# Kernel tuning notes

Hardware: AMD Instinct MI355X
Metric: run time of the kernel (lower is better)

Reference implementation:

```python
import jax, jax.numpy as jnp
import numpy as np

N_NODES = 100000
N_EDGES = 1600000
IN_CH, HID_CH, OUT_CH = 128, 64, 40
NEG_SLOPE = 0.2  # PyG GATConv default LeakyReLU slope


def setup_inputs() -> dict:
    key = jax.random.key(0)
    ks = jax.random.split(key, 12)
    x = jax.random.normal(ks[0], (N_NODES, IN_CH), dtype=jnp.float32)
    src = jax.random.randint(ks[1], (N_EDGES,), 0, N_NODES)
    dst = jax.random.randint(ks[2], (N_EDGES,), 0, N_NODES)
    # remove accidental self loops so that add_remaining_self_loops == append arange
    dst = jnp.where(src == dst, (dst + 1) % N_NODES, dst)
    edge_index = jnp.stack([src, dst], axis=0).astype(jnp.int64)
    s1 = 1.0 / np.sqrt(IN_CH)
    s2 = 1.0 / np.sqrt(HID_CH)
    return {
        "x": x,
        "edge_index": edge_index,
        "W1": jax.random.normal(ks[3], (IN_CH, HID_CH), dtype=jnp.float32) * s1,
        "a_src1": jax.random.normal(ks[4], (HID_CH,), dtype=jnp.float32) * s2,
        "a_dst1": jax.random.normal(ks[5], (HID_CH,), dtype=jnp.float32) * s2,
        "b1": jnp.zeros((HID_CH,), dtype=jnp.float32),
        "W2": jax.random.normal(ks[6], (HID_CH, OUT_CH), dtype=jnp.float32) * s2,
        "a_src2": jax.random.normal(ks[7], (OUT_CH,), dtype=jnp.float32) / np.sqrt(OUT_CH),
        "a_dst2": jax.random.normal(ks[8], (OUT_CH,), dtype=jnp.float32) / np.sqrt(OUT_CH),
        "b2": jnp.zeros((OUT_CH,), dtype=jnp.float32),
    }


def _gat_conv(x, src, dst, W, a_src, a_dst, b, n_nodes):
    # h: [N, F_out] transformed features
    h = x @ W
    # per-node attention logits (heads=1): alpha_src[n] = <h[n], a_src>
    al_src = h @ a_src  # [N]
    al_dst = h @ a_dst  # [N]
    # edge-wise gather + LeakyReLU
    e = al_src[src] + al_dst[dst]          # [E]
    e = jnp.where(e > 0, e, NEG_SLOPE * e)
    # softmax over incoming edges of each destination node
    m = jax.ops.segment_max(e, dst, num_segments=n_nodes)   # [N]
    w = jnp.exp(e - m[dst])                                  # [E]
    z = jax.ops.segment_sum(w, dst, num_segments=n_nodes)    # [N]
    alpha = w / (z[dst] + 1e-16)                              # [E]
    # weighted scatter of neighbor features
    out = jax.ops.segment_sum(h[src] * alpha[:, None], dst, num_segments=n_nodes)
    return out + b


def reference(x, edge_index, W1, a_src1, a_dst1, b1, W2, a_src2, a_dst2, b2):
    n = x.shape[0]
    # add_remaining_self_loops: edges were built with no self loops
    loops = jnp.arange(n, dtype=edge_index.dtype)
    src = jnp.concatenate([edge_index[0], loops])
    dst = jnp.concatenate([edge_index[1], loops])
    h = _gat_conv(x, src, dst, W1, a_src1, a_dst1, b1, n)
    h = jax.nn.relu(h)  # dropout is identity in eval mode
    out = _gat_conv(h, src, dst, W2, a_src2, a_dst2, b2, n)
    return jax.nn.log_softmax(out, axis=1)
```

## Files before the change

kernel.cpp:

```cpp
#include <hip/hip_runtime.h>
#include <hip/hip_fp16.h>

#define N_NODES 100000
#define N_EDGESC 1600000
#define ETOT (N_EDGESC + N_NODES)
#define IN_CH 128
#define HID 64
#define OUTC 40
#define NEG_SLOPE 0.2f
#define BNODES 512
#define NBUCK ((N_NODES + BNODES - 1) / BNODES)
#define BCAP 10240
#define TILE 8192
#define EPT (TILE / 256)
#define NB1 ((ETOT + TILE - 1) / TILE)
#define NG1 ((N_NODES + 127) / 128)

union FusedSmem {
    struct { int hist[256]; int lofs[256]; int gbase[256]; int cur[256]; int stage[TILE]; } b;
    struct { float Ws[IN_CH * HID]; float as_s[HID]; float ad_s[HID]; } g;
};

__global__ __launch_bounds__(256) void fused1_kernel(
    const int* __restrict__ src, const int* __restrict__ dst,
    int* __restrict__ bcur, int* __restrict__ buck,
    const float* __restrict__ x, const float* __restrict__ W1,
    const float* __restrict__ a_src, const float* __restrict__ a_dst,
    __half* __restrict__ h1, float* __restrict__ als, float* __restrict__ ald) {
    __shared__ FusedSmem sm;
    const int t = threadIdx.x;

    if (blockIdx.x < NB1) {
        const int t0 = blockIdx.x * TILE;
        sm.b.hist[t] = 0;
        __syncthreads();

        int payload[EPT];
        int bkt[EPT];
#pragma unroll
        for (int j = 0; j < EPT; j++) {
            int i = t0 + j * 256 + t;
            if (i < ETOT) {
                int s, d;
                if (i < N_EDGESC) { s = src[i]; d = dst[i]; } else { s = d = i - N_EDGESC; }
                int b = d / BNODES;
                bkt[j] = b;
                payload[j] = ((d & (BNODES - 1)) << 17) | s;
                atomicAdd(&sm.b.hist[b], 1);
            } else {
                bkt[j] = -1;
                payload[j] = 0;
            }
        }
        __syncthreads();

        int hv = sm.b.hist[t];
        sm.b.lofs[t] = hv;
        __syncthreads();
        for (int o = 1; o < 256; o <<= 1) {
            int v = (t >= o) ? sm.b.lofs[t - o] : 0;
            __syncthreads();
            sm.b.lofs[t] += v;
            __syncthreads();
        }
        sm.b.cur[t] = sm.b.lofs[t] - hv;
        if (t < NBUCK && hv > 0) sm.b.gbase[t] = t * BCAP + atomicAdd(&bcur[t * 16], hv);
        __syncthreads();

#pragma unroll
        for (int j = 0; j < EPT; j++) {
            if (bkt[j] >= 0) {
                int p = atomicAdd(&sm.b.cur[bkt[j]], 1);
                sm.b.stage[p] = payload[j];
            }
        }
        __syncthreads();

        const int wv = t >> 6;
        const int lane = t & 63;
        for (int b = wv; b < NBUCK; b += 4) {
            int cntb = sm.b.hist[b];
            if (cntb == 0) continue;
            int lo = sm.b.lofs[b] - cntb;
            int gb = sm.b.gbase[b];
            for (int k = lane; k < cntb; k += 64) buck[gb + k] = sm.b.stage[lo + k];
        }
    } else {
        for (int v = t; v < IN_CH * HID; v += 256) sm.g.Ws[v] = W1[v];
        if (t < HID) { sm.g.as_s[t] = a_src[t]; sm.g.ad_s[t] = a_dst[t]; }
        __syncthreads();
        const int n0 = (blockIdx.x - NB1) * 128 + (t >> 2) * 2;
        const int c = t & 3;
        if (n0 >= N_NODES) return;

        float acc0[16], acc1[16];
#pragma unroll
        for (int i = 0; i < 16; i++) { acc0[i] = 0.f; acc1[i] = 0.f; }

        const float4* xr0 = reinterpret_cast<const float4*>(x + (size_t)n0 * IN_CH);
        const float4* xr1 = reinterpret_cast<const float4*>(x + (size_t)(n0 + 1) * IN_CH);
#pragma unroll 2
        for (int kq = 0; kq < IN_CH / 4; kq++) {
            float4 xv0 = xr0[kq];
            float4 xv1 = xr1[kq];
#pragma unroll
            for (int jj = 0; jj < 4; jj++) {
                float xs0 = (jj == 0) ? xv0.x : (jj == 1) ? xv0.y : (jj == 2) ? xv0.z : xv0.w;
                float xs1 = (jj == 0) ? xv1.x : (jj == 1) ? xv1.y : (jj == 2) ? xv1.z : xv1.w;
                const float4* wr = reinterpret_cast<const float4*>(&sm.g.Ws[(kq * 4 + jj) * HID + c * 4]);
#pragma unroll
                for (int j = 0; j < 4; j++) {
                    float4 wv = wr[j * 4];
                    acc0[j * 4 + 0] += xs0 * wv.x; acc1[j * 4 + 0] += xs1 * wv.x;
                    acc0[j * 4 + 1] += xs0 * wv.y; acc1[j * 4 + 1] += xs1 * wv.y;
                    acc0[j * 4 + 2] += xs0 * wv.z; acc1[j * 4 + 2] += xs1 * wv.z;
                    acc0[j * 4 + 3] += xs0 * wv.w; acc1[j * 4 + 3] += xs1 * wv.w;
                }
            }
        }

        float s10 = 0.f, s20 = 0.f, s11 = 0.f, s21 = 0.f;
#pragma unroll
        for (int j = 0; j < 4; j++) {
            int cb = j * 16 + c * 4;
#pragma unroll
            for (int i = 0; i < 4; i++) {
                s10 += acc0[j * 4 + i] * sm.g.as_s[cb + i];
                s20 += acc0[j * 4 + i] * sm.g.ad_s[cb + i];
                s11 += acc1[j * 4 + i] * sm.g.as_s[cb + i];
                s21 += acc1[j * 4 + i] * sm.g.ad_s[cb + i];
            }
            union { __half2 h2[2]; uint2 u; } p0, p1;
            p0.h2[0] = __floats2half2_rn(acc0[j * 4 + 0], acc0[j * 4 + 1]);
            p0.h2[1] = __floats2half2_rn(acc0[j * 4 + 2], acc0[j * 4 + 3]);
            p1.h2[0] = __floats2half2_rn(acc1[j * 4 + 0], acc1[j * 4 + 1]);
            p1.h2[1] = __floats2half2_rn(acc1[j * 4 + 2], acc1[j * 4 + 3]);
            *reinterpret_cast<uint2*>(h1 + (size_t)n0 * HID + cb) = p0.u;
            *reinterpret_cast<uint2*>(h1 + (size_t)(n0 + 1) * HID + cb) = p1.u;
        }
        s10 += __shfl_xor(s10, 1); s10 += __shfl_xor(s10, 2);
        s20 += __shfl_xor(s20, 1); s20 += __shfl_xor(s20, 2);
        s11 += __shfl_xor(s11, 1); s11 += __shfl_xor(s11, 2);
        s21 += __shfl_xor(s21, 1); s21 += __shfl_xor(s21, 2);
        if (c == 0) {
            als[n0] = s10; ald[n0] = s20;
            als[n0 + 1] = s11; ald[n0 + 1] = s21;
        }
    }
}

__global__ __launch_bounds__(256) void bucket2_kernel(const int* __restrict__ bcur,
                                                      const int* __restrict__ buck,
                                                      int* __restrict__ ssrc,
                                                      int* __restrict__ off,
                                                      int* __restrict__ deg) {
    __shared__ int h5[BNODES];
    __shared__ int sdata[256];
    __shared__ int lcur[BNODES];
    const int b = blockIdx.x;
    const int t = threadIdx.x;
    const int base0 = b * BNODES;
    const int bbase = b * BCAP;
    const int cnt_b = bcur[b * 16];

    h5[t] = 0; h5[t + 256] = 0;
    __syncthreads();
    for (int i = t; i < cnt_b; i += 256) atomicAdd(&h5[buck[bbase + i] >> 17], 1);
    __syncthreads();

    int c0 = h5[2 * t], c1 = h5[2 * t + 1];
    int s = c0 + c1;
    sdata[t] = s;
    __syncthreads();
    for (int o = 1; o < 256; o <<= 1) {
        int v = (t >= o) ? sdata[t - o] : 0;
        __syncthreads();
        sdata[t] += v;
        __syncthreads();
    }
    int run = sdata[t] - s;
    int e0 = bbase + run, e1 = bbase + run + c0;
    int n0 = base0 + 2 * t, n1 = n0 + 1;
    if (n0 < N_NODES) { off[n0] = e0; deg[n0] = c0; }
    if (n1 < N_NODES) { off[n1] = e1; deg[n1] = c1; }
    lcur[2 * t] = e0; lcur[2 * t + 1] = e1;
    __syncthreads();

    for (int i = t; i < cnt_b; i += 256) {
        int w = buck[bbase + i];
        int pos = atomicAdd(&lcur[w >> 17], 1);
        ssrc[pos] = w & 0x1FFFF;
    }
}

__global__ __launch_bounds__(256) void gemm2_kernel(
    const __half* __restrict__ hin, const float* __restrict__ W2,
    const float* __restrict__ a_src, const float* __restrict__ a_dst,
    __half* __restrict__ h2, float* __restrict__ als, float* __restrict__ ald) {
    __shared__ float Ws[HID * OUTC];
    __shared__ float as_s[OUTC], ad_s[OUTC];
    for (int v = threadIdx.x; v < HID * OUTC; v += 256) Ws[v] = W2[v];
    if (threadIdx.x < OUTC) { as_s[threadIdx.x] = a_src[threadIdx.x]; ad_s[threadIdx.x] = a_dst[threadIdx.x]; }
    __syncthreads();
    const int t = threadIdx.x;
    const int n0 = blockIdx.x * 128 + (t >> 2) * 2;
    const int c = t & 3;
    if (n0 >= N_NODES) return;

    float acc0[10], acc1[10];
#pragma unroll
    for (int i = 0; i < 10; i++) { acc0[i] = 0.f; acc1[i] = 0.f; }

    const uint4* xr0 = reinterpret_cast<const uint4*>(hin + (size_t)n0 * HID);
    const uint4* xr1 = reinterpret_cast<const uint4*>(hin + (size_t)(n0 + 1) * HID);
#pragma unroll
    for (int kq = 0; kq < HID / 8; kq++) {
        union { uint4 u; __half2 h[4]; } u0, u1;
        u0.u = xr0[kq];
        u1.u = xr1[kq];
        float x0[8], x1[8];
#pragma unroll
        for (int j = 0; j < 4; j++) {
            float2 f0 = __half22float2(u0.h[j]);
            float2 f1 = __half22float2(u1.h[j]);
            x0[2 * j] = f0.x; x0[2 * j + 1] = f0.y;
            x1[2 * j] = f1.x; x1[2 * j + 1] = f1.y;
        }
#pragma unroll
        for (int jj = 0; jj < 8; jj++) {
            float xs0 = x0[jj], xs1 = x1[jj];
            const float2* wr = reinterpret_cast<const float2*>(&Ws[(kq * 8 + jj) * OUTC + c * 2]);
#pragma unroll
            for (int j = 0; j < 5; j++) {
                float2 wv = wr[j * 4];
                acc0[j * 2 + 0] += xs0 * wv.x; acc1[j * 2 + 0] += xs1 * wv.x;
                acc0[j * 2 + 1] += xs0 * wv.y; acc1[j * 2 + 1] += xs1 * wv.y;
            }
        }
    }

    float s10 = 0.f, s20 = 0.f, s11 = 0.f, s21 = 0.f;
#pragma unroll
    for (int j = 0; j < 5; j++) {
        int cb = j * 8 + c * 2;
        s10 += acc0[j * 2 + 0] * as_s[cb] + acc0[j * 2 + 1] * as_s[cb + 1];
        s20 += acc0[j * 2 + 0] * ad_s[cb] + acc0[j * 2 + 1] * ad_s[cb + 1];
        s11 += acc1[j * 2 + 0] * as_s[cb] + acc1[j * 2 + 1] * as_s[cb + 1];
        s21 += acc1[j * 2 + 0] * ad_s[cb] + acc1[j * 2 + 1] * ad_s[cb + 1];
        __half2 p0 = __floats2half2_rn(acc0[j * 2 + 0], acc0[j * 2 + 1]);
        __half2 p1 = __floats2half2_rn(acc1[j * 2 + 0], acc1[j * 2 + 1]);
        *reinterpret_cast<unsigned*>(h2 + (size_t)n0 * OUTC + cb) = *reinterpret_cast<unsigned*>(&p0);
        *reinterpret_cast<unsigned*>(h2 + (size_t)(n0 + 1) * OUTC + cb) = *reinterpret_cast<unsigned*>(&p1);
    }
    s10 += __shfl_xor(s10, 1); s10 += __shfl_xor(s10, 2);
    s20 += __shfl_xor(s20, 1); s20 += __shfl_xor(s20, 2);
    s11 += __shfl_xor(s11, 1); s11 += __shfl_xor(s11, 2);
    s21 += __shfl_xor(s21, 1); s21 += __shfl_xor(s21, 2);
    if (c == 0) {
        als[n0] = s10; ald[n0] = s20;
        als[n0 + 1] = s11; ald[n0 + 1] = s21;
    }
}

__device__ __forceinline__ __half2 shfl_xor_h2(__half2 v, int o) {
    int i = *reinterpret_cast<int*>(&v);
    i = __shfl_xor(i, o);
    return *reinterpret_cast<__half2*>(&i);
}

template <int C, bool FINAL, typename OutT>
__global__ __launch_bounds__(256) void agg_kernel(
    const int* __restrict__ off, const int* __restrict__ degs,
    const int* __restrict__ ssrc,
    const float* __restrict__ als, const float* __restrict__ ald,
    const __half* __restrict__ h, const float* __restrict__ bias,
    OutT* __restrict__ outp) {
    const int lane = threadIdx.x & 63;
    const int d = (blockIdx.x * 256 + threadIdx.x) >> 6;
    if (d >= N_NODES) return;
    const int o0 = off[d];
    const int deg = degs[d];
    const float aldd = ald[d];

    int myS = 0;
    float myW = 0.f;
    if (lane < deg) {
        myS = ssrc[o0 + lane];
        float e = als[myS] + aldd;
        e = e > 0.f ? e : NEG_SLOPE * e;
        myW = __expf(e);
    }

    constexpr int GL = (C + 7) / 8;
    const int g = lane >> 3;
    const int gl = lane & 7;
    const bool lactive = (gl < GL);
    const int dmax = min(deg, 64);

    int ps0 = __shfl(myS, g);
    int ps1 = __shfl(myS, 8 + g);
    int ps2 = __shfl(myS, 16 + g);
    int ps3 = __shfl(myS, 24 + g);
    const bool pv0 = lactive && (g < dmax);
    const bool pv1 = lactive && (8 + g < dmax);
    const bool pv2 = lactive && (16 + g < dmax);
    const bool pv3 = lactive && (24 + g < dmax);
    uint4 P0 = {0, 0, 0, 0}, P1 = P0, P2 = P0, P3 = P0;
    if (pv0) P0 = *reinterpret_cast<const uint4*>(h + (size_t)ps0 * C + 8 * gl);
    if (pv1) P1 = *reinterpret_cast<const uint4*>(h + (size_t)ps1 * C + 8 * gl);
    if (pv2) P2 = *reinterpret_cast<const uint4*>(h + (size_t)ps2 * C + 8 * gl);
    if (pv3) P3 = *reinterpret_cast<const uint4*>(h + (size_t)ps3 * C + 8 * gl);

    float sloc = myW;
    for (int t = 64 + lane; t < deg; t += 64) {
        int s = ssrc[o0 + t];
        float e = als[s] + aldd;
        e = e > 0.f ? e : NEG_SLOPE * e;
        sloc += __expf(e);
    }
#pragma unroll
    for (int o = 32; o; o >>= 1) sloc += __shfl_xor(sloc, o);
    const float inv = 1.0f / (sloc + 1e-16f);
    __half2 mywn2 = __float2half2_rn(myW * inv);
    const int myWbits = *reinterpret_cast<const int*>(&mywn2);

    __half2 a0 = __float2half2_rn(0.f), a1 = a0, a2 = a0, a3 = a0;
    auto fmaP = [&](uint4 u, int wbits) {
        __half2 wn2 = *reinterpret_cast<__half2*>(&wbits);
        union { uint4 u4; __half2 h2[4]; } uu;
        uu.u4 = u;
        a0 = __hfma2(uu.h2[0], wn2, a0);
        a1 = __hfma2(uu.h2[1], wn2, a1);
        a2 = __hfma2(uu.h2[2], wn2, a2);
        a3 = __hfma2(uu.h2[3], wn2, a3);
    };
    auto body = [&](int s, int wbits) {
        uint4 u = *reinterpret_cast<const uint4*>(h + (size_t)s * C + 8 * gl);
        fmaP(u, wbits);
    };

    {
        int w0 = __shfl(myWbits, g);
        int w1 = __shfl(myWbits, 8 + g);
        int w2 = __shfl(myWbits, 16 + g);
        int w3 = __shfl(myWbits, 24 + g);
        if (pv0) fmaP(P0, w0);
        if (pv1) fmaP(P1, w1);
        if (pv2) fmaP(P2, w2);
        if (pv3) fmaP(P3, w3);
    }
    for (int base = 32; base < dmax; base += 16) {
        int t0 = base + g;
        int t1 = base + 8 + g;
        int s0 = __shfl(myS, t0 & 63), w0 = __shfl(myWbits, t0 & 63);
        int s1 = __shfl(myS, t1 & 63), w1 = __shfl(myWbits, t1 & 63);
        if (lactive && t0 < dmax) body(s0, w0);
        if (lactive && t1 < dmax) body(s1, w1);
    }
    for (int t2 = 64 + g; t2 < deg; t2 += 8) {
        int s = ssrc[o0 + t2];
        float e = als[s] + aldd;
        e = e > 0.f ? e : NEG_SLOPE * e;
        __half2 wn2 = __float2half2_rn(__expf(e) * inv);
        if (lactive) body(s, *reinterpret_cast<int*>(&wn2));
    }

#pragma unroll
    for (int o = 8; o <= 32; o <<= 1) {
        a0 = __hadd2(a0, shfl_xor_h2(a0, o));
        a1 = __hadd2(a1, shfl_xor_h2(a1, o));
        a2 = __hadd2(a2, shfl_xor_h2(a2, o));
        a3 = __hadd2(a3, shfl_xor_h2(a3, o));
    }

    const bool valid = (g == 0) && lactive;
    float2 f0 = __half22float2(a0), f1 = __half22float2(a1);
    float2 f2 = __half22float2(a2), f3 = __half22float2(a3);

    if (!FINAL) {
        if (valid) {
            const float4 b0 = reinterpret_cast<const float4*>(bias)[2 * gl];
            const float4 b1 = reinterpret_cast<const float4*>(bias)[2 * gl + 1];
            float v0 = fmaxf(f0.x + b0.x, 0.f), v1 = fmaxf(f0.y + b0.y, 0.f);
            float v2 = fmaxf(f1.x + b0.z, 0.f), v3 = fmaxf(f1.y + b0.w, 0.f);
            float v4 = fmaxf(f2.x + b1.x, 0.f), v5 = fmaxf(f2.y + b1.y, 0.f);
            float v6 = fmaxf(f3.x + b1.z, 0.f), v7 = fmaxf(f3.y + b1.w, 0.f);
            union { __half2 h2[4]; uint4 u; } pk;
            pk.h2[0] = __floats2half2_rn(v0, v1);
            pk.h2[1] = __floats2half2_rn(v2, v3);
            pk.h2[2] = __floats2half2_rn(v4, v5);
            pk.h2[3] = __floats2half2_rn(v6, v7);
            *reinterpret_cast<uint4*>(reinterpret_cast<__half*>(outp) + (size_t)d * C + 8 * gl) = pk.u;
        }
    } else {
        float v[8];
        float mm = -1e30f;
        if (valid) {
            const float4 b0 = reinterpret_cast<const float4*>(bias)[2 * gl];
            const float4 b1 = reinterpret_cast<const float4*>(bias)[2 * gl + 1];
            v[0] = f0.x + b0.x; v[1] = f0.y + b0.y; v[2] = f1.x + b0.z; v[3] = f1.y + b0.w;
            v[4] = f2.x + b1.x; v[5] = f2.y + b1.y; v[6] = f3.x + b1.z; v[7] = f3.y + b1.w;
#pragma unroll
            for (int j = 0; j < 8; j++) mm = fmaxf(mm, v[j]);
        }
#pragma unroll
        for (int o = 1; o <= 4; o <<= 1) mm = fmaxf(mm, __shfl_xor(mm, o));
        float ex = 0.f;
        if (valid) {
#pragma unroll
            for (int j = 0; j < 8; j++) ex += __expf(v[j] - mm);
        }
#pragma unroll
        for (int o = 1; o <= 4; o <<= 1) ex += __shfl_xor(ex, o);
        if (valid) {
            float lse = mm + logf(ex);
            float4 o0v, o1v;
            o0v.x = v[0] - lse; o0v.y = v[1] - lse; o0v.z = v[2] - lse; o0v.w = v[3] - lse;
            o1v.x = v[4] - lse; o1v.y = v[5] - lse; o1v.z = v[6] - lse; o1v.w = v[7] - lse;
            float* orow = reinterpret_cast<float*>(outp) + (size_t)d * C + 8 * gl;
            *reinterpret_cast<float4*>(orow) = o0v;
            *reinterpret_cast<float4*>(orow + 4) = o1v;
        }
    }
}

extern "C" void kernel_launch(void* const* d_in, const int* in_sizes, int n_in,
                              void* d_out, int out_size, void* d_ws, size_t ws_size,
                              hipStream_t stream) {
    const float* x   = (const float*)d_in[0];
    const int*   ei  = (const int*)d_in[1];
    const float* W1  = (const float*)d_in[2];
    const float* as1 = (const float*)d_in[3];
    const float* ad1 = (const float*)d_in[4];
    const float* b1  = (const float*)d_in[5];
    const float* W2  = (const float*)d_in[6];
    const float* as2 = (const float*)d_in[7];
    const float* ad2 = (const float*)d_in[8];
    const float* b2  = (const float*)d_in[9];
    float* out = (float*)d_out;

    char* p = (char*)d_ws;
    auto alloc = [&](size_t bytes) { void* r = p; p += (bytes + 63) & ~(size_t)63; return r; };

    __half* h16 = (__half*)alloc((size_t)N_NODES * 64 * sizeof(__half));
    int* buck   = (int*)alloc((size_t)NBUCK * BCAP * sizeof(int));
    __half* B16 = (__half*)alloc((size_t)N_NODES * 64 * sizeof(__half));
    float* als  = (float*)alloc((size_t)N_NODES * sizeof(float));
    float* ald  = (float*)alloc((size_t)N_NODES * sizeof(float));
    int* off    = (int*)alloc((size_t)N_NODES * sizeof(int));
    int* deg    = (int*)alloc((size_t)N_NODES * sizeof(int));
    int* bcur   = (int*)alloc((size_t)NBUCK * 16 * sizeof(int));
    int* ssrc   = (int*)alloc((size_t)NBUCK * BCAP * sizeof(int));

    const int* srcA = ei;
    const int* dstA = ei + N_EDGESC;

    hipMemsetAsync(bcur, 0, (size_t)NBUCK * 16 * sizeof(int), stream);
    fused1_kernel<<<NB1 + NG1, 256, 0, stream>>>(srcA, dstA, bcur, buck,
                                                 x, W1, as1, ad1, h16, als, ald);
    bucket2_kernel<<<NBUCK, 256, 0, stream>>>(bcur, buck, ssrc, off, deg);

    agg_kernel<HID, false, __half><<<(N_NODES + 3) / 4, 256, 0, stream>>>(
        off, deg, ssrc, als, ald, h16, b1, B16);

    gemm2_kernel<<<(N_NODES + 127) / 128, 256, 0, stream>>>(B16, W2, as2, ad2, h16, als, ald);
    agg_kernel<OUTC, true, float><<<(N_NODES + 3) / 4, 256, 0, stream>>>(
        off, deg, ssrc, als, ald, h16, b2, out);
}
```

Measured before the change: 172.9 us.

## Fuse layer-2 GEMM and attention logits into layer-1 aggregation epilogue

Removes the separate gemm2 kernel. The first aggregation kernel now applies bias and ReLU, multiplies the 64-wide row by W2 held in padded shared memory, and reduces across lanes to write the 40-wide half-precision h2 plus both attention logits. This avoids writing and re-reading the 64-channel hidden activations and drops one launch, at the cost of extra shared memory, shuffles and per-block W2 loading in the aggregation kernel. The bucket kernel also moves to 512 threads per block.

```diff
diff --git a/kernel.cpp b/kernel.cpp
--- a/kernel.cpp
+++ b/kernel.cpp
@@ -149,7 +149,7 @@
     }
 }
 
-__global__ __launch_bounds__(256) void bucket2_kernel(const int* __restrict__ bcur,
+__global__ __launch_bounds__(512) void bucket2_kernel(const int* __restrict__ bcur,
                                                       const int* __restrict__ buck,
                                                       int* __restrict__ ssrc,
                                                       int* __restrict__ off,
@@ -163,102 +163,38 @@
     const int bbase = b * BCAP;
     const int cnt_b = bcur[b * 16];
 
-    h5[t] = 0; h5[t + 256] = 0;
+    h5[t] = 0;
     __syncthreads();
-    for (int i = t; i < cnt_b; i += 256) atomicAdd(&h5[buck[bbase + i] >> 17], 1);
+    for (int i = t; i < cnt_b; i += 512) atomicAdd(&h5[buck[bbase + i] >> 17], 1);
     __syncthreads();
 
-    int c0 = h5[2 * t], c1 = h5[2 * t + 1];
-    int s = c0 + c1;
-    sdata[t] = s;
+    int c0 = 0, c1 = 0, s = 0;
+    if (t < 256) {
+        c0 = h5[2 * t]; c1 = h5[2 * t + 1];
+        s = c0 + c1;
+        sdata[t] = s;
+    }
     __syncthreads();
     for (int o = 1; o < 256; o <<= 1) {
-        int v = (t >= o) ? sdata[t - o] : 0;
-        __syncthreads();
-        sdata[t] += v;
-        __syncthreads();
-    }
-    int run = sdata[t] - s;
-    int e0 = bbase + run, e1 = bbase + run + c0;
-    int n0 = base0 + 2 * t, n1 = n0 + 1;
-    if (n0 < N_NODES) { off[n0] = e0; deg[n0] = c0; }
-    if (n1 < N_NODES) { off[n1] = e1; deg[n1] = c1; }
-    lcur[2 * t] = e0; lcur[2 * t + 1] = e1;
+        int v = (t < 256 && t >= o) ? sdata[t - o] : 0;
+        __syncthreads();
+        if (t < 256) sdata[t] += v;
+        __syncthreads();
+    }
+    if (t < 256) {
+        int run = sdata[t] - s;
+        int e0 = bbase + run, e1 = bbase + run + c0;
+        int n0 = base0 + 2 * t, n1 = n0 + 1;
+        if (n0 < N_NODES) { off[n0] = e0; deg[n0] = c0; }
+        if (n1 < N_NODES) { off[n1] = e1; deg[n1] = c1; }
+        lcur[2 * t] = e0; lcur[2 * t + 1] = e1;
+    }
     __syncthreads();
 
-    for (int i = t; i < cnt_b; i += 256) {
+    for (int i = t; i < cnt_b; i += 512) {
         int w = buck[bbase + i];
         int pos = atomicAdd(&lcur[w >> 17], 1);
         ssrc[pos] = w & 0x1FFFF;
-    }
-}
-
-__global__ __launch_bounds__(256) void gemm2_kernel(
-    const __half* __restrict__ hin, const float* __restrict__ W2,
-    const float* __restrict__ a_src, const float* __restrict__ a_dst,
-    __half* __restrict__ h2, float* __restrict__ als, float* __restrict__ ald) {
-    __shared__ float Ws[HID * OUTC];
-    __shared__ float as_s[OUTC], ad_s[OUTC];
-    for (int v = threadIdx.x; v < HID * OUTC; v += 256) Ws[v] = W2[v];
-    if (threadIdx.x < OUTC) { as_s[threadIdx.x] = a_src[threadIdx.x]; ad_s[threadIdx.x] = a_dst[threadIdx.x]; }
-    __syncthreads();
-    const int t = threadIdx.x;
-    const int n0 = blockIdx.x * 128 + (t >> 2) * 2;
-    const int c = t & 3;
-    if (n0 >= N_NODES) return;
-
-    float acc0[10], acc1[10];
-#pragma unroll
-    for (int i = 0; i < 10; i++) { acc0[i] = 0.f; acc1[i] = 0.f; }
-
-    const uint4* xr0 = reinterpret_cast<const uint4*>(hin + (size_t)n0 * HID);
-    const uint4* xr1 = reinterpret_cast<const uint4*>(hin + (size_t)(n0 + 1) * HID);
-#pragma unroll
-    for (int kq = 0; kq < HID / 8; kq++) {
-        union { uint4 u; __half2 h[4]; } u0, u1;
-        u0.u = xr0[kq];
-        u1.u = xr1[kq];
-        float x0[8], x1[8];
-#pragma unroll
-        for (int j = 0; j < 4; j++) {
-            float2 f0 = __half22float2(u0.h[j]);
-            float2 f1 = __half22float2(u1.h[j]);
-            x0[2 * j] = f0.x; x0[2 * j + 1] = f0.y;
-            x1[2 * j] = f1.x; x1[2 * j + 1] = f1.y;
-        }
-#pragma unroll
-        for (int jj = 0; jj < 8; jj++) {
-            float xs0 = x0[jj], xs1 = x1[jj];
-            const float2* wr = reinterpret_cast<const float2*>(&Ws[(kq * 8 + jj) * OUTC + c * 2]);
-#pragma unroll
-            for (int j = 0; j < 5; j++) {
-                float2 wv = wr[j * 4];
-                acc0[j * 2 + 0] += xs0 * wv.x; acc1[j * 2 + 0] += xs1 * wv.x;
-                acc0[j * 2 + 1] += xs0 * wv.y; acc1[j * 2 + 1] += xs1 * wv.y;
-            }
-        }
-    }
-
-    float s10 = 0.f, s20 = 0.f, s11 = 0.f, s21 = 0.f;
-#pragma unroll
-    for (int j = 0; j < 5; j++) {
-        int cb = j * 8 + c * 2;
-        s10 += acc0[j * 2 + 0] * as_s[cb] + acc0[j * 2 + 1] * as_s[cb + 1];
-        s20 += acc0[j * 2 + 0] * ad_s[cb] + acc0[j * 2 + 1] * ad_s[cb + 1];
-        s11 += acc1[j * 2 + 0] * as_s[cb] + acc1[j * 2 + 1] * as_s[cb + 1];
-        s21 += acc1[j * 2 + 0] * ad_s[cb] + acc1[j * 2 + 1] * ad_s[cb + 1];
-        __half2 p0 = __floats2half2_rn(acc0[j * 2 + 0], acc0[j * 2 + 1]);
-        __half2 p1 = __floats2half2_rn(acc1[j * 2 + 0], acc1[j * 2 + 1]);
-        *reinterpret_cast<unsigned*>(h2 + (size_t)n0 * OUTC + cb) = *reinterpret_cast<unsigned*>(&p0);
-        *reinterpret_cast<unsigned*>(h2 + (size_t)(n0 + 1) * OUTC + cb) = *reinterpret_cast<unsigned*>(&p1);
-    }
-    s10 += __shfl_xor(s10, 1); s10 += __shfl_xor(s10, 2);
-    s20 += __shfl_xor(s20, 1); s20 += __shfl_xor(s20, 2);
-    s11 += __shfl_xor(s11, 1); s11 += __shfl_xor(s11, 2);
-    s21 += __shfl_xor(s21, 1); s21 += __shfl_xor(s21, 2);
-    if (c == 0) {
-        als[n0] = s10; ald[n0] = s20;
-        als[n0 + 1] = s11; ald[n0 + 1] = s21;
     }
 }
 
@@ -268,13 +204,26 @@
     return *reinterpret_cast<__half2*>(&i);
 }
 
-template <int C, bool FINAL, typename OutT>
+template <int C, int MODE, typename OutT>
 __global__ __launch_bounds__(256) void agg_kernel(
     const int* __restrict__ off, const int* __restrict__ degs,
     const int* __restrict__ ssrc,
     const float* __restrict__ als, const float* __restrict__ ald,
     const __half* __restrict__ h, const float* __restrict__ bias,
-    OutT* __restrict__ outp) {
+    const float* __restrict__ W2, const float* __restrict__ as2, const float* __restrict__ ad2,
+    OutT* __restrict__ outp, float* __restrict__ als_o, float* __restrict__ ald_o) {
+    __shared__ float Ws2[(MODE == 0) ? (64 * 41) : 1];
+    __shared__ float a2s[(MODE == 0) ? 40 : 1];
+    __shared__ float a2d[(MODE == 0) ? 40 : 1];
+    if (MODE == 0) {
+        for (int v = threadIdx.x; v < HID * OUTC; v += 256) {
+            int k = v / OUTC, j = v - k * OUTC;
+            Ws2[k * 41 + j] = W2[v];
+        }
+        if (threadIdx.x < OUTC) { a2s[threadIdx.x] = as2[threadIdx.x]; a2d[threadIdx.x] = ad2[threadIdx.x]; }
+        __syncthreads();
+    }
+
     const int lane = threadIdx.x & 63;
     const int d = (blockIdx.x * 256 + threadIdx.x) >> 6;
     if (d >= N_NODES) return;
@@ -373,33 +322,56 @@
         a3 = __hadd2(a3, shfl_xor_h2(a3, o));
     }
 
-    const bool valid = (g == 0) && lactive;
     float2 f0 = __half22float2(a0), f1 = __half22float2(a1);
     float2 f2 = __half22float2(a2), f3 = __half22float2(a3);
 
-    if (!FINAL) {
-        if (valid) {
-            const float4 b0 = reinterpret_cast<const float4*>(bias)[2 * gl];
-            const float4 b1 = reinterpret_cast<const float4*>(bias)[2 * gl + 1];
-            float v0 = fmaxf(f0.x + b0.x, 0.f), v1 = fmaxf(f0.y + b0.y, 0.f);
-            float v2 = fmaxf(f1.x + b0.z, 0.f), v3 = fmaxf(f1.y + b0.w, 0.f);
-            float v4 = fmaxf(f2.x + b1.x, 0.f), v5 = fmaxf(f2.y + b1.y, 0.f);
-            float v6 = fmaxf(f3.x + b1.z, 0.f), v7 = fmaxf(f3.y + b1.w, 0.f);
-            union { __half2 h2[4]; uint4 u; } pk;
-            pk.h2[0] = __floats2half2_rn(v0, v1);
-            pk.h2[1] = __floats2half2_rn(v2, v3);
-            pk.h2[2] = __floats2half2_rn(v4, v5);
-            pk.h2[3] = __floats2half2_rn(v6, v7);
-            *reinterpret_cast<uint4*>(reinterpret_cast<__half*>(outp) + (size_t)d * C + 8 * gl) = pk.u;
+    if (MODE == 0) {
+        const float4 b0 = reinterpret_cast<const float4*>(bias)[2 * gl];
+        const float4 b1v = reinterpret_cast<const float4*>(bias)[2 * gl + 1];
+        float v[8];
+        v[0] = fmaxf(f0.x + b0.x, 0.f); v[1] = fmaxf(f0.y + b0.y, 0.f);
+        v[2] = fmaxf(f1.x + b0.z, 0.f); v[3] = fmaxf(f1.y + b0.w, 0.f);
+        v[4] = fmaxf(f2.x + b1v.x, 0.f); v[5] = fmaxf(f2.y + b1v.y, 0.f);
+        v[6] = fmaxf(f3.x + b1v.z, 0.f); v[7] = fmaxf(f3.y + b1v.w, 0.f);
+        float part[5];
+#pragma unroll
+        for (int jj = 0; jj < 5; jj++) part[jj] = 0.f;
+#pragma unroll
+        for (int i = 0; i < 8; i++) {
+            const float* wrow = &Ws2[(8 * gl + i) * 41 + 5 * g];
+#pragma unroll
+            for (int jj = 0; jj < 5; jj++) part[jj] += v[i] * wrow[jj];
+        }
+#pragma unroll
+        for (int o = 1; o <= 4; o <<= 1) {
+#pragma unroll
+            for (int jj = 0; jj < 5; jj++) part[jj] += __shfl_xor(part[jj], o);
+        }
+        float p1 = 0.f, p2 = 0.f;
+        if (gl == 0) {
+#pragma unroll
+            for (int jj = 0; jj < 5; jj++) {
+                p1 += part[jj] * a2s[5 * g + jj];
+                p2 += part[jj] * a2d[5 * g + jj];
+            }
+        }
+#pragma unroll
+        for (int o = 8; o <= 32; o <<= 1) { p1 += __shfl_xor(p1, o); p2 += __shfl_xor(p2, o); }
+        if (lane == 0) { als_o[d] = p1; ald_o[d] = p2; }
+        if (gl == 0) {
+            __half* orow = reinterpret_cast<__half*>(outp) + (size_t)d * OUTC + 5 * g;
+#pragma unroll
+            for (int jj = 0; jj < 5; jj++) orow[jj] = __float2half(part[jj]);
         }
     } else {
+        const bool valid = (g == 0) && lactive;
         float v[8];
         float mm = -1e30f;
         if (valid) {
             const float4 b0 = reinterpret_cast<const float4*>(bias)[2 * gl];
-            const float4 b1 = reinterpret_cast<const float4*>(bias)[2 * gl + 1];
+            const float4 b1v = reinterpret_cast<const float4*>(bias)[2 * gl + 1];
             v[0] = f0.x + b0.x; v[1] = f0.y + b0.y; v[2] = f1.x + b0.z; v[3] = f1.y + b0.w;
-            v[4] = f2.x + b1.x; v[5] = f2.y + b1.y; v[6] = f3.x + b1.z; v[7] = f3.y + b1.w;
+            v[4] = f2.x + b1v.x; v[5] = f2.y + b1v.y; v[6] = f3.x + b1v.z; v[7] = f3.y + b1v.w;
 #pragma unroll
             for (int j = 0; j < 8; j++) mm = fmaxf(mm, v[j]);
         }
@@ -447,6 +419,8 @@
     __half* B16 = (__half*)alloc((size_t)N_NODES * 64 * sizeof(__half));
     float* als  = (float*)alloc((size_t)N_NODES * sizeof(float));
     float* ald  = (float*)alloc((size_t)N_NODES * sizeof(float));
+    float* als_b = (float*)alloc((size_t)N_NODES * sizeof(float));
+    float* ald_b = (float*)alloc((size_t)N_NODES * sizeof(float));
     int* off    = (int*)alloc((size_t)N_NODES * sizeof(int));
     int* deg    = (int*)alloc((size_t)N_NODES * sizeof(int));
     int* bcur   = (int*)alloc((size_t)NBUCK * 16 * sizeof(int));
@@ -458,12 +432,11 @@
     hipMemsetAsync(bcur, 0, (size_t)NBUCK * 16 * sizeof(int), stream);
     fused1_kernel<<<NB1 + NG1, 256, 0, stream>>>(srcA, dstA, bcur, buck,
                                                  x, W1, as1, ad1, h16, als, ald);
-    bucket2_kernel<<<NBUCK, 256, 0, stream>>>(bcur, buck, ssrc, off, deg);
-
-    agg_kernel<HID, false, __half><<<(N_NODES + 3) / 4, 256, 0, stream>>>(
-        off, deg, ssrc, als, ald, h16, b1, B16);
-
-    gemm2_kernel<<<(N_NODES + 127) / 128, 256, 0, stream>>>(B16, W2, as2, ad2, h16, als, ald);
-    agg_kernel<OUTC, true, float><<<(N_NODES + 3) / 4, 256, 0, stream>>>(
-        off, deg, ssrc, als, ald, h16, b2, out);
+    bucket2_kernel<<<NBUCK, 512, 0, stream>>>(bcur, buck, ssrc, off, deg);
+
+    agg_kernel<HID, 0, __half><<<(N_NODES + 3) / 4, 256, 0, stream>>>(
+        off, deg, ssrc, als, ald, h16, b1, W2, as2, ad2, B16, als_b, ald_b);
+
+    agg_kernel<OUTC, 1, float><<<(N_NODES + 3) / 4, 256, 0, stream>>>(
+        off, deg, ssrc, als_b, ald_b, B16, b2, nullptr, nullptr, nullptr, out, nullptr, nullptr);
 }
```

After: 199.6 us. +15.4%, slower.
